# Kernel optimization log

Hardware: AMD Instinct MI355X
Metric: run time of the kernel (lower is better)

Reference implementation:

```python
import jax, jax.numpy as jnp
import numpy as np

ALPHA = 0.2  # LeakyReLU negative slope


def setup_inputs() -> dict:
    key = jax.random.key(0)
    k_x, k_w, k_a = jax.random.split(key, 3)
    B, N, F_in = 4, 2048, 128
    H, nhid = 4, 32  # out_channel=128, nheads=4
    x = jax.random.normal(k_x, (B, N, F_in), dtype=jnp.float32)
    # per-head projection and attention vector, xavier-ish scale
    W = jax.random.normal(k_w, (H, F_in, nhid), dtype=jnp.float32) * (1.414 * np.sqrt(2.0 / (F_in + nhid))) / np.sqrt(3.0) * np.sqrt(3.0)
    a = jax.random.normal(k_a, (H, 2 * nhid), dtype=jnp.float32) * (1.414 * np.sqrt(2.0 / (2 * nhid + 1)))
    return {"x": x, "W": W, "a": a}


def reference(x, W, a):
    # x: [B,N,F_in], W: [H,F_in,d], a: [H,2d]
    H = W.shape[0]
    d = W.shape[2]
    B, N, _ = x.shape
    Wh = jnp.einsum('bni,hij->bhnj', x, W)          # [B,H,N,d]
    a1 = a[:, :d]                                    # [H,d]
    a2 = a[:, d:]                                    # [H,d]
    Wh1 = jnp.einsum('bhnd,hd->bhn', Wh, a1)         # [B,H,N]
    Wh2 = jnp.einsum('bhnd,hd->bhn', Wh, a2)         # [B,H,N]
    e = Wh1[:, :, :, None] + Wh2[:, :, None, :]      # [B,H,N,N]
    e = jnp.where(e > 0, e, ALPHA * e)               # LeakyReLU
    attn = jax.nn.softmax(e, axis=-1)                # softmax over source nodes
    h = jnp.einsum('bhij,bhjd->bhid', attn, Wh)      # [B,H,N,d]
    h = jax.nn.elu(h)
    # concat heads along feature dim: [B,N,H*d]
    out = jnp.transpose(h, (0, 2, 1, 3)).reshape(B, N, H * d)
    return out
```

## Files before the change

### kernel.cpp

```cpp
#include <hip/hip_runtime.h>


#define LOG2E 1.4426950408889634f
constexpr int Nn = 2048, Fin = 128, Dd = 32;

typedef _Float16 half8 __attribute__((ext_vector_type(8)));
typedef _Float16 half4v __attribute__((ext_vector_type(4)));
typedef _Float16 half2v __attribute__((ext_vector_type(2)));
typedef float f32x4 __attribute__((ext_vector_type(4)));

union H8 { half2v h2[4]; half8 h8; };

__global__ __launch_bounds__(256) void k1_wh(
    const float* __restrict__ x, const float* __restrict__ W,
    const float* __restrict__ a, _Float16* __restrict__ whT,
    float* __restrict__ sArr, float* __restrict__ tArr) {
  int blk = blockIdx.x;
  int bh = blk >> 5, tile = blk & 31;
  int b = bh >> 2, h = bh & 3;
  int tid = threadIdx.x, w = tid >> 6, lane = tid & 63;
  int q = lane >> 4, m = lane & 15;
  int rowbase = tile * 64 + w * 16;

  const float* Wq = W + h * Fin * Dd;
  const float* xb = x + (size_t)(b * Nn + rowbase + m) * Fin;

  f32x4 acc[2];
  acc[0] = (f32x4){0.f, 0.f, 0.f, 0.f};
  acc[1] = (f32x4){0.f, 0.f, 0.f, 0.f};

#pragma unroll
  for (int kt = 0; kt < 4; ++kt) {
    float4 x0 = *(const float4*)(xb + kt * 32 + q * 8);
    float4 x1 = *(const float4*)(xb + kt * 32 + q * 8 + 4);
    float xv[8] = {x0.x, x0.y, x0.z, x0.w, x1.x, x1.y, x1.z, x1.w};
    half8 Ah, Al;
#pragma unroll
    for (int j = 0; j < 8; ++j) {
      _Float16 hi = (_Float16)xv[j];
      Ah[j] = hi;
      Al[j] = (_Float16)(xv[j] - (float)hi);
    }
#pragma unroll
    for (int nt = 0; nt < 2; ++nt) {
      half8 Bh, Bl;
#pragma unroll
      for (int j = 0; j < 8; ++j) {
        float wv = Wq[(kt * 32 + q * 8 + j) * Dd + nt * 16 + m];
        _Float16 hi = (_Float16)wv;
        Bh[j] = hi;
        Bl[j] = (_Float16)(wv - (float)hi);
      }
      acc[nt] = __builtin_amdgcn_mfma_f32_16x16x32_f16(Ah, Bh, acc[nt], 0, 0, 0);
      acc[nt] = __builtin_amdgcn_mfma_f32_16x16x32_f16(Al, Bh, acc[nt], 0, 0, 0);
      acc[nt] = __builtin_amdgcn_mfma_f32_16x16x32_f16(Ah, Bl, acc[nt], 0, 0, 0);
    }
  }

#pragma unroll
  for (int nt = 0; nt < 2; ++nt) {
    int d = nt * 16 + m;
    half4v h4;
#pragma unroll
    for (int r = 0; r < 4; ++r) h4[r] = (_Float16)acc[nt][r];
    *(half4v*)(whT + (size_t)(bh * Dd + d) * Nn + rowbase + q * 4) = h4;
  }

  const float* ah = a + h * 2 * Dd;
  float a1m0 = ah[m], a1m1 = ah[16 + m];
  float a2m0 = ah[Dd + m], a2m1 = ah[Dd + 16 + m];
#pragma unroll
  for (int r = 0; r < 4; ++r) {
    float ps = acc[0][r] * a1m0 + acc[1][r] * a1m1;
    float pt = acc[0][r] * a2m0 + acc[1][r] * a2m1;
#pragma unroll
    for (int off = 1; off < 16; off <<= 1) {
      ps += __shfl_xor(ps, off);
      pt += __shfl_xor(pt, off);
    }
    if (m == 0) {
      sArr[bh * Nn + rowbase + q * 4 + r] = ps;
      tArr[bh * Nn + rowbase + q * 4 + r] = pt;
    }
  }
}

__global__ __launch_bounds__(256) void k3_attn(
    const _Float16* __restrict__ whT, const float* __restrict__ sArr,
    const float* __restrict__ tArr, float* __restrict__ out) {
  __shared__ float smem[4 * 64 * 33 + 256];
  _Float16* Ef = (_Float16*)smem;
  _Float16* Ff = (_Float16*)(smem + 1024);
  float* red = smem + 2048;

  int blk = blockIdx.x;
  int bh = blk >> 5, tile = blk & 31;
  int b = bh >> 2, h = bh & 3;
  int tid = threadIdx.x, w = tid >> 6, lane = tid & 63;
  int q = lane >> 4, m = lane & 15;

  float tv[8];
  float mx = -1e30f;
#pragma unroll
  for (int k = 0; k < 8; ++k) {
    tv[k] = tArr[bh * Nn + tid + k * 256];
    mx = fmaxf(mx, tv[k]);
  }
  red[tid] = mx;
  __syncthreads();
  for (int ss = 128; ss > 0; ss >>= 1) {
    if (tid < ss) red[tid] = fmaxf(red[tid], red[tid + ss]);
    __syncthreads();
  }
  float T = red[0];
  __syncthreads();
#pragma unroll
  for (int k = 0; k < 8; ++k) {
    float dt = tv[k] - T;
    Ef[tid + k * 256] = (_Float16)__builtin_amdgcn_exp2f(LOG2E * dt);
    Ff[tid + k * 256] = (_Float16)__builtin_amdgcn_exp2f(0.2f * LOG2E * dt);
  }

  half2v aa[4], bb[4];
#pragma unroll
  for (int t = 0; t < 4; ++t) {
    float es = sArr[bh * Nn + tile * 64 + t * 16 + m] + T;
    float al = __builtin_amdgcn_exp2f(0.8f * LOG2E * fminf(es, 0.f));
    float be = __builtin_amdgcn_exp2f(-0.8f * LOG2E * fmaxf(es, 0.f));
    _Float16 ah_ = (_Float16)al, bh_ = (_Float16)be;
    aa[t] = (half2v){ah_, ah_};
    bb[t] = (half2v){bh_, bh_};
  }
  __syncthreads();

  f32x4 acc[4][2];
#pragma unroll
  for (int t = 0; t < 4; ++t) {
    acc[t][0] = (f32x4){0.f, 0.f, 0.f, 0.f};
    acc[t][1] = (f32x4){0.f, 0.f, 0.f, 0.f};
  }
  float den[4] = {0.f, 0.f, 0.f, 0.f};
  const half2v ones = (half2v){(_Float16)1.f, (_Float16)1.f};

  const _Float16* wb = whT + (size_t)bh * Dd * Nn;

  for (int s = 0; s < 16; ++s) {
    int jb = w * 512 + s * 32;
    half8 B0 = *(const half8*)(wb + (size_t)m * Nn + jb + q * 8);
    half8 B1 = *(const half8*)(wb + (size_t)(16 + m) * Nn + jb + q * 8);
    H8 E, F;
    E.h8 = *(const half8*)&Ef[jb + q * 8];
    F.h8 = *(const half8*)&Ff[jb + q * 8];

#pragma unroll
    for (int t = 0; t < 4; ++t) {
      H8 P;
#pragma unroll
      for (int kk = 0; kk < 4; ++kk) {
        half2v pe = aa[t] * E.h2[kk];
        half2v pf = bb[t] * F.h2[kk];
        half2v p2 = __builtin_elementwise_max(pe, pf);
        P.h2[kk] = p2;
        den[t] = __builtin_amdgcn_fdot2(p2, ones, den[t], false);
      }
      acc[t][0] = __builtin_amdgcn_mfma_f32_16x16x32_f16(P.h8, B0, acc[t][0], 0, 0, 0);
      acc[t][1] = __builtin_amdgcn_mfma_f32_16x16x32_f16(P.h8, B1, acc[t][1], 0, 0, 0);
    }
  }

#pragma unroll
  for (int t = 0; t < 4; ++t) {
    den[t] += __shfl_xor(den[t], 16);
    den[t] += __shfl_xor(den[t], 32);
  }
  __syncthreads();
  float* redN = smem;
  float* redD = smem + 4 * 64 * 33;
#pragma unroll
  for (int t = 0; t < 4; ++t) {
#pragma unroll
    for (int dh = 0; dh < 2; ++dh)
#pragma unroll
      for (int r = 0; r < 4; ++r)
        redN[(w * 64 + t * 16 + q * 4 + r) * 33 + dh * 16 + m] = acc[t][dh][r];
    if (q == 0) redD[w * 64 + t * 16 + m] = den[t];
  }
  __syncthreads();
  {
    int rl = tid >> 2, dg = (tid & 3) * 8;
    float num[8];
#pragma unroll
    for (int i = 0; i < 8; ++i)
      num[i] = redN[(0 * 64 + rl) * 33 + dg + i] + redN[(1 * 64 + rl) * 33 + dg + i] +
               redN[(2 * 64 + rl) * 33 + dg + i] + redN[(3 * 64 + rl) * 33 + dg + i];
    float dt = redD[rl] + redD[64 + rl] + redD[128 + rl] + redD[192 + rl];
    float rd = 1.0f / dt;
    float* orow = out + (size_t)(b * Nn + tile * 64 + rl) * (4 * Dd) + h * Dd + dg;
#pragma unroll
    for (int i = 0; i < 8; ++i) {
      float hv = num[i] * rd;
      num[i] = hv > 0.f ? hv : (__builtin_amdgcn_exp2f(hv * LOG2E) - 1.0f);
    }
    *(float4*)orow = make_float4(num[0], num[1], num[2], num[3]);
    *((float4*)orow + 1) = make_float4(num[4], num[5], num[6], num[7]);
  }
}

extern "C" void kernel_launch(void* const* d_in, const int* in_sizes, int n_in,
                              void* d_out, int out_size, void* d_ws, size_t ws_size,
                              hipStream_t stream) {
  const float* x = (const float*)d_in[0];
  const float* W = (const float*)d_in[1];
  const float* a = (const float*)d_in[2];
  float* out = (float*)d_out;

  float* wsf = (float*)d_ws;
  float* sArr = wsf;
  float* tArr = sArr + 32768;
  _Float16* whT = (_Float16*)(tArr + 32768);

  k1_wh<<<dim3(512), dim3(256), 0, stream>>>(x, W, a, whT, sArr, tArr);
  k3_attn<<<dim3(512), dim3(256), 0, stream>>>(whT, sArr, tArr, out);
}
```

Measured before the change: 77.38 us.

## Give each attention wave full source range and drop cross-wave LDS reduction

The attention kernel is reorganized so each wave owns 16 target rows and sweeps all 2048 source nodes. This removes the split-K partial sums across four waves and the large LDS reduction buffer, and uses 128-thread blocks on a grid twice as large. The softmax denominator is now computed with an extra MFMA against a ones vector instead of fdot2, and the next whT slice is prefetched into registers. The projection kernel now stages W in LDS and issues the x loads up front. In exchange, each wave reloads whT for every row tile, so total L2/global traffic for whT rises roughly fourfold, and MFMA work per useful output grows.

Result: slower. 101.6 us (+31.3%).

```diff
diff --git a/kernel.cpp b/kernel.cpp
--- a/kernel.cpp
+++ b/kernel.cpp
@@ -15,6 +15,7 @@
     const float* __restrict__ x, const float* __restrict__ W,
     const float* __restrict__ a, _Float16* __restrict__ whT,
     float* __restrict__ sArr, float* __restrict__ tArr) {
+  __shared__ float Wlds[Fin][Dd + 1];
   int blk = blockIdx.x;
   int bh = blk >> 5, tile = blk & 31;
   int b = bh >> 2, h = bh & 3;
@@ -22,8 +23,26 @@
   int q = lane >> 4, m = lane & 15;
   int rowbase = tile * 64 + w * 16;
 
-  const float* Wq = W + h * Fin * Dd;
+  {
+    const float4* src = (const float4*)(W + h * Fin * Dd);
+#pragma unroll
+    for (int r = 0; r < 4; ++r) {
+      float4 v = src[tid + r * 256];
+      int e = (tid + r * 256) * 4;
+      Wlds[e >> 5][e & 31] = v.x;
+      Wlds[(e + 1) >> 5][(e + 1) & 31] = v.y;
+      Wlds[(e + 2) >> 5][(e + 2) & 31] = v.z;
+      Wlds[(e + 3) >> 5][(e + 3) & 31] = v.w;
+    }
+  }
   const float* xb = x + (size_t)(b * Nn + rowbase + m) * Fin;
+  float4 xl[8];
+#pragma unroll
+  for (int kt = 0; kt < 4; ++kt) {
+    xl[2 * kt] = *(const float4*)(xb + kt * 32 + q * 8);
+    xl[2 * kt + 1] = *(const float4*)(xb + kt * 32 + q * 8 + 4);
+  }
+  __syncthreads();
 
   f32x4 acc[2];
   acc[0] = (f32x4){0.f, 0.f, 0.f, 0.f};
@@ -31,9 +50,8 @@
 
 #pragma unroll
   for (int kt = 0; kt < 4; ++kt) {
-    float4 x0 = *(const float4*)(xb + kt * 32 + q * 8);
-    float4 x1 = *(const float4*)(xb + kt * 32 + q * 8 + 4);
-    float xv[8] = {x0.x, x0.y, x0.z, x0.w, x1.x, x1.y, x1.z, x1.w};
+    float xv[8] = {xl[2 * kt].x, xl[2 * kt].y, xl[2 * kt].z, xl[2 * kt].w,
+                   xl[2 * kt + 1].x, xl[2 * kt + 1].y, xl[2 * kt + 1].z, xl[2 * kt + 1].w};
     half8 Ah, Al;
 #pragma unroll
     for (int j = 0; j < 8; ++j) {
@@ -46,7 +64,7 @@
       half8 Bh, Bl;
 #pragma unroll
       for (int j = 0; j < 8; ++j) {
-        float wv = Wq[(kt * 32 + q * 8 + j) * Dd + nt * 16 + m];
+        float wv = Wlds[kt * 32 + q * 8 + j][nt * 16 + m];
         _Float16 hi = (_Float16)wv;
         Bh[j] = hi;
         Bl[j] = (_Float16)(wv - (float)hi);
@@ -85,124 +103,81 @@
   }
 }
 
-__global__ __launch_bounds__(256) void k3_attn(
+__global__ __launch_bounds__(128) void k3_attn(
     const _Float16* __restrict__ whT, const float* __restrict__ sArr,
     const float* __restrict__ tArr, float* __restrict__ out) {
-  __shared__ float smem[4 * 64 * 33 + 256];
-  _Float16* Ef = (_Float16*)smem;
-  _Float16* Ff = (_Float16*)(smem + 1024);
-  float* red = smem + 2048;
-
+  __shared__ _Float16 Ef[Nn], Ff[Nn];
+  __shared__ float red[2];
   int blk = blockIdx.x;
-  int bh = blk >> 5, tile = blk & 31;
+  int bh = blk >> 6, tp = blk & 63;
   int b = bh >> 2, h = bh & 3;
   int tid = threadIdx.x, w = tid >> 6, lane = tid & 63;
   int q = lane >> 4, m = lane & 15;
+  int rowbase = (tp * 2 + w) * 16;
 
-  float tv[8];
+  float tv[16];
   float mx = -1e30f;
 #pragma unroll
-  for (int k = 0; k < 8; ++k) {
-    tv[k] = tArr[bh * Nn + tid + k * 256];
+  for (int k = 0; k < 16; ++k) {
+    tv[k] = tArr[bh * Nn + tid + k * 128];
     mx = fmaxf(mx, tv[k]);
   }
-  red[tid] = mx;
+#pragma unroll
+  for (int off = 1; off < 64; off <<= 1) mx = fmaxf(mx, __shfl_xor(mx, off));
+  if (lane == 0) red[w] = mx;
   __syncthreads();
-  for (int ss = 128; ss > 0; ss >>= 1) {
-    if (tid < ss) red[tid] = fmaxf(red[tid], red[tid + ss]);
-    __syncthreads();
+  float T = fmaxf(red[0], red[1]);
+#pragma unroll
+  for (int k = 0; k < 16; ++k) {
+    float dt = tv[k] - T;
+    Ef[tid + k * 128] = (_Float16)__builtin_amdgcn_exp2f(LOG2E * dt);
+    Ff[tid + k * 128] = (_Float16)__builtin_amdgcn_exp2f(0.2f * LOG2E * dt);
   }
-  float T = red[0];
-  __syncthreads();
-#pragma unroll
-  for (int k = 0; k < 8; ++k) {
-    float dt = tv[k] - T;
-    Ef[tid + k * 256] = (_Float16)__builtin_amdgcn_exp2f(LOG2E * dt);
-    Ff[tid + k * 256] = (_Float16)__builtin_amdgcn_exp2f(0.2f * LOG2E * dt);
-  }
-
-  half2v aa[4], bb[4];
-#pragma unroll
-  for (int t = 0; t < 4; ++t) {
-    float es = sArr[bh * Nn + tile * 64 + t * 16 + m] + T;
-    float al = __builtin_amdgcn_exp2f(0.8f * LOG2E * fminf(es, 0.f));
-    float be = __builtin_amdgcn_exp2f(-0.8f * LOG2E * fmaxf(es, 0.f));
-    _Float16 ah_ = (_Float16)al, bh_ = (_Float16)be;
-    aa[t] = (half2v){ah_, ah_};
-    bb[t] = (half2v){bh_, bh_};
-  }
+  float es = sArr[bh * Nn + rowbase + m] + T;
+  float al = __builtin_amdgcn_exp2f(0.8f * LOG2E * fminf(es, 0.f));
+  float be = __builtin_amdgcn_exp2f(-0.8f * LOG2E * fmaxf(es, 0.f));
+  half2v aa = (half2v){(_Float16)al, (_Float16)al};
+  half2v bb = (half2v){(_Float16)be, (_Float16)be};
   __syncthreads();
 
-  f32x4 acc[4][2];
+  f32x4 acc0 = (f32x4){0.f, 0.f, 0.f, 0.f};
+  f32x4 acc1 = (f32x4){0.f, 0.f, 0.f, 0.f};
+  f32x4 accD = (f32x4){0.f, 0.f, 0.f, 0.f};
+  const _Float16 one = (_Float16)1.f;
+  const half8 ONES = (half8){one, one, one, one, one, one, one, one};
+
+  const _Float16* r0 = whT + (size_t)(bh * Dd + m) * Nn + q * 8;
+  const _Float16* r1 = whT + (size_t)(bh * Dd + 16 + m) * Nn + q * 8;
+
+  half8 nB0 = *(const half8*)r0;
+  half8 nB1 = *(const half8*)r1;
+  for (int s = 0; s < 64; ++s) {
+    half8 B0 = nB0, B1 = nB1;
+    int jn = (s + 1) * 32;
+    nB0 = *(const half8*)(r0 + jn);
+    nB1 = *(const half8*)(r1 + jn);
+    H8 E, F, P;
+    E.h8 = *(const half8*)&Ef[s * 32 + q * 8];
+    F.h8 = *(const half8*)&Ff[s * 32 + q * 8];
 #pragma unroll
-  for (int t = 0; t < 4; ++t) {
-    acc[t][0] = (f32x4){0.f, 0.f, 0.f, 0.f};
-    acc[t][1] = (f32x4){0.f, 0.f, 0.f, 0.f};
-  }
-  float den[4] = {0.f, 0.f, 0.f, 0.f};
-  const half2v ones = (half2v){(_Float16)1.f, (_Float16)1.f};
-
-  const _Float16* wb = whT + (size_t)bh * Dd * Nn;
-
-  for (int s = 0; s < 16; ++s) {
-    int jb = w * 512 + s * 32;
-    half8 B0 = *(const half8*)(wb + (size_t)m * Nn + jb + q * 8);
-    half8 B1 = *(const half8*)(wb + (size_t)(16 + m) * Nn + jb + q * 8);
-    H8 E, F;
-    E.h8 = *(const half8*)&Ef[jb + q * 8];
-    F.h8 = *(const half8*)&Ff[jb + q * 8];
-
-#pragma unroll
-    for (int t = 0; t < 4; ++t) {
-      H8 P;
-#pragma unroll
-      for (int kk = 0; kk < 4; ++kk) {
-        half2v pe = aa[t] * E.h2[kk];
-        half2v pf = bb[t] * F.h2[kk];
-        half2v p2 = __builtin_elementwise_max(pe, pf);
-        P.h2[kk] = p2;
-        den[t] = __builtin_amdgcn_fdot2(p2, ones, den[t], false);
-      }
-      acc[t][0] = __builtin_amdgcn_mfma_f32_16x16x32_f16(P.h8, B0, acc[t][0], 0, 0, 0);
-      acc[t][1] = __builtin_amdgcn_mfma_f32_16x16x32_f16(P.h8, B1, acc[t][1], 0, 0, 0);
-    }
+    for (int kk = 0; kk < 4; ++kk)
+      P.h2[kk] = __builtin_elementwise_max(aa * E.h2[kk], bb * F.h2[kk]);
+    acc0 = __builtin_amdgcn_mfma_f32_16x16x32_f16(P.h8, B0, acc0, 0, 0, 0);
+    acc1 = __builtin_amdgcn_mfma_f32_16x16x32_f16(P.h8, B1, acc1, 0, 0, 0);
+    accD = __builtin_amdgcn_mfma_f32_16x16x32_f16(P.h8, ONES, accD, 0, 0, 0);
   }
 
 #pragma unroll
-  for (int t = 0; t < 4; ++t) {
-    den[t] += __shfl_xor(den[t], 16);
-    den[t] += __shfl_xor(den[t], 32);
-  }
-  __syncthreads();
-  float* redN = smem;
-  float* redD = smem + 4 * 64 * 33;
-#pragma unroll
-  for (int t = 0; t < 4; ++t) {
-#pragma unroll
-    for (int dh = 0; dh < 2; ++dh)
-#pragma unroll
-      for (int r = 0; r < 4; ++r)
-        redN[(w * 64 + t * 16 + q * 4 + r) * 33 + dh * 16 + m] = acc[t][dh][r];
-    if (q == 0) redD[w * 64 + t * 16 + m] = den[t];
-  }
-  __syncthreads();
-  {
-    int rl = tid >> 2, dg = (tid & 3) * 8;
-    float num[8];
-#pragma unroll
-    for (int i = 0; i < 8; ++i)
-      num[i] = redN[(0 * 64 + rl) * 33 + dg + i] + redN[(1 * 64 + rl) * 33 + dg + i] +
-               redN[(2 * 64 + rl) * 33 + dg + i] + redN[(3 * 64 + rl) * 33 + dg + i];
-    float dt = redD[rl] + redD[64 + rl] + redD[128 + rl] + redD[192 + rl];
-    float rd = 1.0f / dt;
-    float* orow = out + (size_t)(b * Nn + tile * 64 + rl) * (4 * Dd) + h * Dd + dg;
-#pragma unroll
-    for (int i = 0; i < 8; ++i) {
-      float hv = num[i] * rd;
-      num[i] = hv > 0.f ? hv : (__builtin_amdgcn_exp2f(hv * LOG2E) - 1.0f);
-    }
-    *(float4*)orow = make_float4(num[0], num[1], num[2], num[3]);
-    *((float4*)orow + 1) = make_float4(num[4], num[5], num[6], num[7]);
+  for (int r = 0; r < 4; ++r) {
+    int row = rowbase + q * 4 + r;
+    float rd = 1.0f / accD[r];
+    float* orow = out + (size_t)(b * Nn + row) * (4 * Dd) + h * Dd;
+    float v0 = acc0[r] * rd;
+    float v1 = acc1[r] * rd;
+    v0 = v0 > 0.f ? v0 : (__builtin_amdgcn_exp2f(v0 * LOG2E) - 1.0f);
+    v1 = v1 > 0.f ? v1 : (__builtin_amdgcn_exp2f(v1 * LOG2E) - 1.0f);
+    orow[m] = v0;
+    orow[16 + m] = v1;
   }
 }
 
@@ -220,5 +195,5 @@
   _Float16* whT = (_Float16*)(tArr + 32768);
 
   k1_wh<<<dim3(512), dim3(256), 0, stream>>>(x, W, a, whT, sArr, tArr);
-  k3_attn<<<dim3(512), dim3(256), 0, stream>>>(whT, sArr, tArr, out);
+  k3_attn<<<dim3(1024), dim3(128), 0, stream>>>(whT, sArr, tArr, out);
 }
```

## Split attention across 8 waves, MFMA denominator, prefetch Wh, precompute W fragments

Applied to the files above, without the earlier changes.

The attention kernel grows to 512 threads, so each wave covers 256 source nodes instead of 512, with the cross-wave reduction widened to match. The softmax denominator is now accumulated by an extra MFMA against a ones vector instead of per-lane fdot2 plus shuffles, and Wh fragments are double-buffered in registers. A new small kernel splits W into fp16 hi/lo fragments once, so the projection kernel loads them directly, and its x loads are hoisted ahead of the loop. The cost is an extra launch, more shared memory per block, and prefetch loads that read past each wave's range.

New measurement: 78.21 us. No clear change (+1.1%).

```diff
diff --git a/kernel.cpp b/kernel.cpp
--- a/kernel.cpp
+++ b/kernel.cpp
@@ -11,8 +11,28 @@
 
 union H8 { half2v h2[4]; half8 h8; };
 
+__global__ __launch_bounds__(256) void k0_wfrag(
+    const float* __restrict__ W, _Float16* __restrict__ Wf) {
+  int t = blockIdx.x * 256 + threadIdx.x;
+  int h = t >> 9, rem = t & 511;
+  int kt = rem >> 7, rem2 = rem & 127;
+  int nt = rem2 >> 6, lane = rem2 & 63;
+  int q = lane >> 4, m = lane & 15;
+  const float* Wh_ = W + h * Fin * Dd;
+  half8 hi8, lo8;
+#pragma unroll
+  for (int j = 0; j < 8; ++j) {
+    float wv = Wh_[(kt * 32 + q * 8 + j) * Dd + nt * 16 + m];
+    _Float16 hi = (_Float16)wv;
+    hi8[j] = hi;
+    lo8[j] = (_Float16)(wv - (float)hi);
+  }
+  *(half8*)(Wf + (size_t)t * 16) = hi8;
+  *(half8*)(Wf + (size_t)t * 16 + 8) = lo8;
+}
+
 __global__ __launch_bounds__(256) void k1_wh(
-    const float* __restrict__ x, const float* __restrict__ W,
+    const float* __restrict__ x, const _Float16* __restrict__ Wf,
     const float* __restrict__ a, _Float16* __restrict__ whT,
     float* __restrict__ sArr, float* __restrict__ tArr) {
   int blk = blockIdx.x;
@@ -22,8 +42,13 @@
   int q = lane >> 4, m = lane & 15;
   int rowbase = tile * 64 + w * 16;
 
-  const float* Wq = W + h * Fin * Dd;
   const float* xb = x + (size_t)(b * Nn + rowbase + m) * Fin;
+  float4 xl[8];
+#pragma unroll
+  for (int kt = 0; kt < 4; ++kt) {
+    xl[2 * kt] = *(const float4*)(xb + kt * 32 + q * 8);
+    xl[2 * kt + 1] = *(const float4*)(xb + kt * 32 + q * 8 + 4);
+  }
 
   f32x4 acc[2];
   acc[0] = (f32x4){0.f, 0.f, 0.f, 0.f};
@@ -31,9 +56,8 @@
 
 #pragma unroll
   for (int kt = 0; kt < 4; ++kt) {
-    float4 x0 = *(const float4*)(xb + kt * 32 + q * 8);
-    float4 x1 = *(const float4*)(xb + kt * 32 + q * 8 + 4);
-    float xv[8] = {x0.x, x0.y, x0.z, x0.w, x1.x, x1.y, x1.z, x1.w};
+    float xv[8] = {xl[2 * kt].x, xl[2 * kt].y, xl[2 * kt].z, xl[2 * kt].w,
+                   xl[2 * kt + 1].x, xl[2 * kt + 1].y, xl[2 * kt + 1].z, xl[2 * kt + 1].w};
     half8 Ah, Al;
 #pragma unroll
     for (int j = 0; j < 8; ++j) {
@@ -43,14 +67,9 @@
     }
 #pragma unroll
     for (int nt = 0; nt < 2; ++nt) {
-      half8 Bh, Bl;
-#pragma unroll
-      for (int j = 0; j < 8; ++j) {
-        float wv = Wq[(kt * 32 + q * 8 + j) * Dd + nt * 16 + m];
-        _Float16 hi = (_Float16)wv;
-        Bh[j] = hi;
-        Bl[j] = (_Float16)(wv - (float)hi);
-      }
+      size_t fo = (size_t)((((h * 4 + kt) * 2 + nt) * 64) + lane) * 16;
+      half8 Bh = *(const half8*)(Wf + fo);
+      half8 Bl = *(const half8*)(Wf + fo + 8);
       acc[nt] = __builtin_amdgcn_mfma_f32_16x16x32_f16(Ah, Bh, acc[nt], 0, 0, 0);
       acc[nt] = __builtin_amdgcn_mfma_f32_16x16x32_f16(Al, Bh, acc[nt], 0, 0, 0);
       acc[nt] = __builtin_amdgcn_mfma_f32_16x16x32_f16(Ah, Bl, acc[nt], 0, 0, 0);
@@ -85,10 +104,10 @@
   }
 }
 
-__global__ __launch_bounds__(256) void k3_attn(
+__global__ __launch_bounds__(512) void k3_attn(
     const _Float16* __restrict__ whT, const float* __restrict__ sArr,
     const float* __restrict__ tArr, float* __restrict__ out) {
-  __shared__ float smem[4 * 64 * 33 + 256];
+  __shared__ float smem[8 * 64 * 33 + 512];
   _Float16* Ef = (_Float16*)smem;
   _Float16* Ff = (_Float16*)(smem + 1024);
   float* red = smem + 2048;
@@ -99,83 +118,80 @@
   int tid = threadIdx.x, w = tid >> 6, lane = tid & 63;
   int q = lane >> 4, m = lane & 15;
 
-  float tv[8];
+  float tv[4];
   float mx = -1e30f;
 #pragma unroll
-  for (int k = 0; k < 8; ++k) {
-    tv[k] = tArr[bh * Nn + tid + k * 256];
+  for (int k = 0; k < 4; ++k) {
+    tv[k] = tArr[bh * Nn + tid + k * 512];
     mx = fmaxf(mx, tv[k]);
   }
   red[tid] = mx;
   __syncthreads();
-  for (int ss = 128; ss > 0; ss >>= 1) {
+  for (int ss = 256; ss > 0; ss >>= 1) {
     if (tid < ss) red[tid] = fmaxf(red[tid], red[tid + ss]);
     __syncthreads();
   }
   float T = red[0];
-  __syncthreads();
-#pragma unroll
-  for (int k = 0; k < 8; ++k) {
+#pragma unroll
+  for (int k = 0; k < 4; ++k) {
     float dt = tv[k] - T;
-    Ef[tid + k * 256] = (_Float16)__builtin_amdgcn_exp2f(LOG2E * dt);
-    Ff[tid + k * 256] = (_Float16)__builtin_amdgcn_exp2f(0.2f * LOG2E * dt);
-  }
-
+    Ef[tid + k * 512] = (_Float16)__builtin_amdgcn_exp2f(LOG2E * dt);
+    Ff[tid + k * 512] = (_Float16)__builtin_amdgcn_exp2f(0.2f * LOG2E * dt);
+  }
   half2v aa[4], bb[4];
 #pragma unroll
   for (int t = 0; t < 4; ++t) {
     float es = sArr[bh * Nn + tile * 64 + t * 16 + m] + T;
     float al = __builtin_amdgcn_exp2f(0.8f * LOG2E * fminf(es, 0.f));
     float be = __builtin_amdgcn_exp2f(-0.8f * LOG2E * fmaxf(es, 0.f));
-    _Float16 ah_ = (_Float16)al, bh_ = (_Float16)be;
-    aa[t] = (half2v){ah_, ah_};
-    bb[t] = (half2v){bh_, bh_};
-  }
-  __syncthreads();
-
-  f32x4 acc[4][2];
+    aa[t] = (half2v){(_Float16)al, (_Float16)al};
+    bb[t] = (half2v){(_Float16)be, (_Float16)be};
+  }
+  __syncthreads();
+
+  f32x4 acc[4][2], accD[4];
 #pragma unroll
   for (int t = 0; t < 4; ++t) {
     acc[t][0] = (f32x4){0.f, 0.f, 0.f, 0.f};
     acc[t][1] = (f32x4){0.f, 0.f, 0.f, 0.f};
-  }
-  float den[4] = {0.f, 0.f, 0.f, 0.f};
-  const half2v ones = (half2v){(_Float16)1.f, (_Float16)1.f};
-
-  const _Float16* wb = whT + (size_t)bh * Dd * Nn;
-
-  for (int s = 0; s < 16; ++s) {
-    int jb = w * 512 + s * 32;
-    half8 B0 = *(const half8*)(wb + (size_t)m * Nn + jb + q * 8);
-    half8 B1 = *(const half8*)(wb + (size_t)(16 + m) * Nn + jb + q * 8);
+    accD[t] = (f32x4){0.f, 0.f, 0.f, 0.f};
+  }
+  const _Float16 one = (_Float16)1.f;
+  const half8 ONES = (half8){one, one, one, one, one, one, one, one};
+
+  const _Float16* r0 = whT + (size_t)(bh * Dd + m) * Nn;
+  const _Float16* r1 = whT + (size_t)(bh * Dd + 16 + m) * Nn;
+  int jw = w * 256 + q * 8;
+
+  half8 pB0[2], pB1[2];
+  pB0[0] = *(const half8*)(r0 + jw);
+  pB1[0] = *(const half8*)(r1 + jw);
+  pB0[1] = *(const half8*)(r0 + jw + 32);
+  pB1[1] = *(const half8*)(r1 + jw + 32);
+
+  for (int s = 0; s < 8; ++s) {
+    half8 B0 = pB0[s & 1], B1 = pB1[s & 1];
+    int jn = jw + (s + 2) * 32;
+    pB0[s & 1] = *(const half8*)(r0 + jn);
+    pB1[s & 1] = *(const half8*)(r1 + jn);
     H8 E, F;
-    E.h8 = *(const half8*)&Ef[jb + q * 8];
-    F.h8 = *(const half8*)&Ff[jb + q * 8];
-
+    E.h8 = *(const half8*)&Ef[w * 256 + s * 32 + q * 8];
+    F.h8 = *(const half8*)&Ff[w * 256 + s * 32 + q * 8];
 #pragma unroll
     for (int t = 0; t < 4; ++t) {
       H8 P;
 #pragma unroll
-      for (int kk = 0; kk < 4; ++kk) {
-        half2v pe = aa[t] * E.h2[kk];
-        half2v pf = bb[t] * F.h2[kk];
-        half2v p2 = __builtin_elementwise_max(pe, pf);
-        P.h2[kk] = p2;
-        den[t] = __builtin_amdgcn_fdot2(p2, ones, den[t], false);
-      }
+      for (int kk = 0; kk < 4; ++kk)
+        P.h2[kk] = __builtin_elementwise_max(aa[t] * E.h2[kk], bb[t] * F.h2[kk]);
       acc[t][0] = __builtin_amdgcn_mfma_f32_16x16x32_f16(P.h8, B0, acc[t][0], 0, 0, 0);
       acc[t][1] = __builtin_amdgcn_mfma_f32_16x16x32_f16(P.h8, B1, acc[t][1], 0, 0, 0);
-    }
-  }
-
-#pragma unroll
-  for (int t = 0; t < 4; ++t) {
-    den[t] += __shfl_xor(den[t], 16);
-    den[t] += __shfl_xor(den[t], 32);
-  }
+      accD[t] = __builtin_amdgcn_mfma_f32_16x16x32_f16(P.h8, ONES, accD[t], 0, 0, 0);
+    }
+  }
+
   __syncthreads();
   float* redN = smem;
-  float* redD = smem + 4 * 64 * 33;
+  float* redD = smem + 8 * 64 * 33;
 #pragma unroll
   for (int t = 0; t < 4; ++t) {
 #pragma unroll
@@ -183,26 +199,29 @@
 #pragma unroll
       for (int r = 0; r < 4; ++r)
         redN[(w * 64 + t * 16 + q * 4 + r) * 33 + dh * 16 + m] = acc[t][dh][r];
-    if (q == 0) redD[w * 64 + t * 16 + m] = den[t];
+    if (m == 0)
+#pragma unroll
+      for (int r = 0; r < 4; ++r) redD[w * 64 + t * 16 + q * 4 + r] = accD[t][r];
   }
   __syncthreads();
   {
-    int rl = tid >> 2, dg = (tid & 3) * 8;
-    float num[8];
-#pragma unroll
-    for (int i = 0; i < 8; ++i)
-      num[i] = redN[(0 * 64 + rl) * 33 + dg + i] + redN[(1 * 64 + rl) * 33 + dg + i] +
-               redN[(2 * 64 + rl) * 33 + dg + i] + redN[(3 * 64 + rl) * 33 + dg + i];
-    float dt = redD[rl] + redD[64 + rl] + redD[128 + rl] + redD[192 + rl];
+    int rl = tid >> 3, c4 = (tid & 7) * 4;
+    float num[4] = {0.f, 0.f, 0.f, 0.f};
+    float dt = 0.f;
+#pragma unroll
+    for (int ww = 0; ww < 8; ++ww) {
+      dt += redD[ww * 64 + rl];
+#pragma unroll
+      for (int i = 0; i < 4; ++i) num[i] += redN[(ww * 64 + rl) * 33 + c4 + i];
+    }
     float rd = 1.0f / dt;
-    float* orow = out + (size_t)(b * Nn + tile * 64 + rl) * (4 * Dd) + h * Dd + dg;
-#pragma unroll
-    for (int i = 0; i < 8; ++i) {
+    float* orow = out + (size_t)(b * Nn + tile * 64 + rl) * (4 * Dd) + h * Dd + c4;
+#pragma unroll
+    for (int i = 0; i < 4; ++i) {
       float hv = num[i] * rd;
       num[i] = hv > 0.f ? hv : (__builtin_amdgcn_exp2f(hv * LOG2E) - 1.0f);
     }
     *(float4*)orow = make_float4(num[0], num[1], num[2], num[3]);
-    *((float4*)orow + 1) = make_float4(num[4], num[5], num[6], num[7]);
   }
 }
 
@@ -218,7 +237,9 @@
   float* sArr = wsf;
   float* tArr = sArr + 32768;
   _Float16* whT = (_Float16*)(tArr + 32768);
-
-  k1_wh<<<dim3(512), dim3(256), 0, stream>>>(x, W, a, whT, sArr, tArr);
-  k3_attn<<<dim3(512), dim3(256), 0, stream>>>(whT, sArr, tArr, out);
-}
+  _Float16* Wf = whT + (size_t)16 * Dd * Nn;
+
+  k0_wfrag<<<dim3(8), dim3(256), 0, stream>>>(W, Wf);
+  k1_wh<<<dim3(512), dim3(256), 0, stream>>>(x, Wf, a, whT, sArr, tArr);
+  k3_attn<<<dim3(512), dim3(512), 0, stream>>>(whT, sArr, tArr, out);
+}
```

## Prefetch Wh tiles, compute softmax denominator via MFMA, stage W in LDS

Applied to the files above, without the earlier changes.

In the attention kernel, the Wh B-operands are double-buffered in registers, loading two steps ahead. The per-row softmax denominator now comes from an extra MFMA against a ones vector instead of per-lane fdot2 accumulation and shuffles, and one redundant barrier is removed. In the projection kernel, the per-head W matrix is staged in padded LDS and the x loads are hoisted ahead of the barrier. This trades more MFMA work and some over-read past each wave's slice on the last prefetches for less VALU work and better latency hiding.

After: 111.7 us. +44.3%, slower.

```diff
diff --git a/kernel.cpp b/kernel.cpp
--- a/kernel.cpp
+++ b/kernel.cpp
@@ -15,6 +15,7 @@
     const float* __restrict__ x, const float* __restrict__ W,
     const float* __restrict__ a, _Float16* __restrict__ whT,
     float* __restrict__ sArr, float* __restrict__ tArr) {
+  __shared__ float Wlds[Fin][Dd + 1];
   int blk = blockIdx.x;
   int bh = blk >> 5, tile = blk & 31;
   int b = bh >> 2, h = bh & 3;
@@ -22,8 +23,26 @@
   int q = lane >> 4, m = lane & 15;
   int rowbase = tile * 64 + w * 16;
 
-  const float* Wq = W + h * Fin * Dd;
+  {
+    const float4* src = (const float4*)(W + h * Fin * Dd);
+#pragma unroll
+    for (int r = 0; r < 4; ++r) {
+      float4 v = src[tid + r * 256];
+      int e = (tid + r * 256) * 4;
+      Wlds[e >> 5][e & 31] = v.x;
+      Wlds[(e + 1) >> 5][(e + 1) & 31] = v.y;
+      Wlds[(e + 2) >> 5][(e + 2) & 31] = v.z;
+      Wlds[(e + 3) >> 5][(e + 3) & 31] = v.w;
+    }
+  }
   const float* xb = x + (size_t)(b * Nn + rowbase + m) * Fin;
+  float4 xl[8];
+#pragma unroll
+  for (int kt = 0; kt < 4; ++kt) {
+    xl[2 * kt] = *(const float4*)(xb + kt * 32 + q * 8);
+    xl[2 * kt + 1] = *(const float4*)(xb + kt * 32 + q * 8 + 4);
+  }
+  __syncthreads();
 
   f32x4 acc[2];
   acc[0] = (f32x4){0.f, 0.f, 0.f, 0.f};
@@ -31,9 +50,8 @@
 
 #pragma unroll
   for (int kt = 0; kt < 4; ++kt) {
-    float4 x0 = *(const float4*)(xb + kt * 32 + q * 8);
-    float4 x1 = *(const float4*)(xb + kt * 32 + q * 8 + 4);
-    float xv[8] = {x0.x, x0.y, x0.z, x0.w, x1.x, x1.y, x1.z, x1.w};
+    float xv[8] = {xl[2 * kt].x, xl[2 * kt].y, xl[2 * kt].z, xl[2 * kt].w,
+                   xl[2 * kt + 1].x, xl[2 * kt + 1].y, xl[2 * kt + 1].z, xl[2 * kt + 1].w};
     half8 Ah, Al;
 #pragma unroll
     for (int j = 0; j < 8; ++j) {
@@ -46,7 +64,7 @@
       half8 Bh, Bl;
 #pragma unroll
       for (int j = 0; j < 8; ++j) {
-        float wv = Wq[(kt * 32 + q * 8 + j) * Dd + nt * 16 + m];
+        float wv = Wlds[kt * 32 + q * 8 + j][nt * 16 + m];
         _Float16 hi = (_Float16)wv;
         Bh[j] = hi;
         Bl[j] = (_Float16)(wv - (float)hi);
@@ -113,66 +131,63 @@
     __syncthreads();
   }
   float T = red[0];
-  __syncthreads();
 #pragma unroll
   for (int k = 0; k < 8; ++k) {
     float dt = tv[k] - T;
     Ef[tid + k * 256] = (_Float16)__builtin_amdgcn_exp2f(LOG2E * dt);
     Ff[tid + k * 256] = (_Float16)__builtin_amdgcn_exp2f(0.2f * LOG2E * dt);
   }
-
   half2v aa[4], bb[4];
 #pragma unroll
   for (int t = 0; t < 4; ++t) {
     float es = sArr[bh * Nn + tile * 64 + t * 16 + m] + T;
     float al = __builtin_amdgcn_exp2f(0.8f * LOG2E * fminf(es, 0.f));
     float be = __builtin_amdgcn_exp2f(-0.8f * LOG2E * fmaxf(es, 0.f));
-    _Float16 ah_ = (_Float16)al, bh_ = (_Float16)be;
-    aa[t] = (half2v){ah_, ah_};
-    bb[t] = (half2v){bh_, bh_};
-  }
-  __syncthreads();
-
-  f32x4 acc[4][2];
+    aa[t] = (half2v){(_Float16)al, (_Float16)al};
+    bb[t] = (half2v){(_Float16)be, (_Float16)be};
+  }
+  __syncthreads();
+
+  f32x4 acc[4][2], accD[4];
 #pragma unroll
   for (int t = 0; t < 4; ++t) {
     acc[t][0] = (f32x4){0.f, 0.f, 0.f, 0.f};
     acc[t][1] = (f32x4){0.f, 0.f, 0.f, 0.f};
-  }
-  float den[4] = {0.f, 0.f, 0.f, 0.f};
-  const half2v ones = (half2v){(_Float16)1.f, (_Float16)1.f};
-
-  const _Float16* wb = whT + (size_t)bh * Dd * Nn;
+    accD[t] = (f32x4){0.f, 0.f, 0.f, 0.f};
+  }
+  const _Float16 one = (_Float16)1.f;
+  const half8 ONES = (half8){one, one, one, one, one, one, one, one};
+
+  const _Float16* r0 = whT + (size_t)(bh * Dd + m) * Nn;
+  const _Float16* r1 = whT + (size_t)(bh * Dd + 16 + m) * Nn;
+  int jw = w * 512 + q * 8;
+
+  half8 pB0[2], pB1[2];
+  pB0[0] = *(const half8*)(r0 + jw);
+  pB1[0] = *(const half8*)(r1 + jw);
+  pB0[1] = *(const half8*)(r0 + jw + 32);
+  pB1[1] = *(const half8*)(r1 + jw + 32);
 
   for (int s = 0; s < 16; ++s) {
-    int jb = w * 512 + s * 32;
-    half8 B0 = *(const half8*)(wb + (size_t)m * Nn + jb + q * 8);
-    half8 B1 = *(const half8*)(wb + (size_t)(16 + m) * Nn + jb + q * 8);
+    half8 B0 = pB0[s & 1], B1 = pB1[s & 1];
+    int jn = jw + (s + 2) * 32;
+    pB0[s & 1] = *(const half8*)(r0 + jn);
+    pB1[s & 1] = *(const half8*)(r1 + jn);
     H8 E, F;
-    E.h8 = *(const half8*)&Ef[jb + q * 8];
-    F.h8 = *(const half8*)&Ff[jb + q * 8];
-
+    E.h8 = *(const half8*)&Ef[w * 512 + s * 32 + q * 8];
+    F.h8 = *(const half8*)&Ff[w * 512 + s * 32 + q * 8];
 #pragma unroll
     for (int t = 0; t < 4; ++t) {
       H8 P;
 #pragma unroll
-      for (int kk = 0; kk < 4; ++kk) {
-        half2v pe = aa[t] * E.h2[kk];
-        half2v pf = bb[t] * F.h2[kk];
-        half2v p2 = __builtin_elementwise_max(pe, pf);
-        P.h2[kk] = p2;
-        den[t] = __builtin_amdgcn_fdot2(p2, ones, den[t], false);
-      }
+      for (int kk = 0; kk < 4; ++kk)
+        P.h2[kk] = __builtin_elementwise_max(aa[t] * E.h2[kk], bb[t] * F.h2[kk]);
       acc[t][0] = __builtin_amdgcn_mfma_f32_16x16x32_f16(P.h8, B0, acc[t][0], 0, 0, 0);
       acc[t][1] = __builtin_amdgcn_mfma_f32_16x16x32_f16(P.h8, B1, acc[t][1], 0, 0, 0);
-    }
-  }
-
-#pragma unroll
-  for (int t = 0; t < 4; ++t) {
-    den[t] += __shfl_xor(den[t], 16);
-    den[t] += __shfl_xor(den[t], 32);
-  }
+      accD[t] = __builtin_amdgcn_mfma_f32_16x16x32_f16(P.h8, ONES, accD[t], 0, 0, 0);
+    }
+  }
+
   __syncthreads();
   float* redN = smem;
   float* redD = smem + 4 * 64 * 33;
@@ -183,17 +198,23 @@
 #pragma unroll
       for (int r = 0; r < 4; ++r)
         redN[(w * 64 + t * 16 + q * 4 + r) * 33 + dh * 16 + m] = acc[t][dh][r];
-    if (q == 0) redD[w * 64 + t * 16 + m] = den[t];
+    if (m == 0)
+#pragma unroll
+      for (int r = 0; r < 4; ++r) redD[w * 64 + t * 16 + q * 4 + r] = accD[t][r];
   }
   __syncthreads();
   {
     int rl = tid >> 2, dg = (tid & 3) * 8;
     float num[8];
-#pragma unroll
-    for (int i = 0; i < 8; ++i)
-      num[i] = redN[(0 * 64 + rl) * 33 + dg + i] + redN[(1 * 64 + rl) * 33 + dg + i] +
-               redN[(2 * 64 + rl) * 33 + dg + i] + redN[(3 * 64 + rl) * 33 + dg + i];
-    float dt = redD[rl] + redD[64 + rl] + redD[128 + rl] + redD[192 + rl];
+    float dt = 0.f;
+#pragma unroll
+    for (int i = 0; i < 8; ++i) num[i] = 0.f;
+#pragma unroll
+    for (int ww = 0; ww < 4; ++ww) {
+      dt += redD[ww * 64 + rl];
+#pragma unroll
+      for (int i = 0; i < 8; ++i) num[i] += redN[(ww * 64 + rl) * 33 + dg + i];
+    }
     float rd = 1.0f / dt;
     float* orow = out + (size_t)(b * Nn + tile * 64 + rl) * (4 * Dd) + h * Dd + dg;
 #pragma unroll
```
